# Performance work log

Measured on AMD Instinct MI355X. Metric: run time of the kernel, lower is better.

## Reference

```python
import jax, jax.numpy as jnp
import numpy as np

N = 50000
E = 500000
R = 8
IN_DIM = 128
HID = 128
NUM_CLASSES = 16
NUM_GRAPHS = 64


def setup_inputs() -> dict:
    key = jax.random.key(0)
    ks = jax.random.split(key, 12)
    x = jax.random.normal(ks[0], (N, IN_DIM), dtype=jnp.float32)
    edge_index = jax.random.randint(ks[1], (2, E), 0, N)
    edge_type = jax.random.randint(ks[2], (E,), 0, R)
    batch = jnp.sort(jax.random.randint(ks[3], (N,), 0, NUM_GRAPHS))
    s = 1.0 / np.sqrt(IN_DIM)
    W1 = jax.random.uniform(ks[4], (R, IN_DIM, HID), minval=-s, maxval=s, dtype=jnp.float32)
    root1 = jax.random.uniform(ks[5], (IN_DIM, HID), minval=-s, maxval=s, dtype=jnp.float32)
    b1 = jnp.zeros((HID,), jnp.float32)
    s2 = 1.0 / np.sqrt(HID)
    W2 = jax.random.uniform(ks[6], (R, HID, HID), minval=-s2, maxval=s2, dtype=jnp.float32)
    root2 = jax.random.uniform(ks[7], (HID, HID), minval=-s2, maxval=s2, dtype=jnp.float32)
    b2 = jnp.zeros((HID,), jnp.float32)
    linW = jax.random.uniform(ks[8], (HID, NUM_CLASSES), minval=-s2, maxval=s2, dtype=jnp.float32)
    linb = jnp.zeros((NUM_CLASSES,), jnp.float32)
    return {"x": x, "edge_index": edge_index, "edge_type": edge_type, "batch": batch,
            "W1": W1, "root1": root1, "b1": b1, "W2": W2, "root2": root2, "b2": b2,
            "linW": linW, "linb": linb}


def rgcn_conv(x, src, dst, rel, W, root, b):
    # Per-relation transform of ALL nodes once: [R, N, H] (avoids per-edge weight gather)
    xW = jnp.einsum('nd,rdh->rnh', x, W)
    msg = xW[rel, src]                      # [E, H] gather per edge
    # PyG RGCNConv default aggr='mean': mean over neighbors per (dst, relation)
    seg = dst * R + rel                     # composite segment id
    cnt = jax.ops.segment_sum(jnp.ones((msg.shape[0],), msg.dtype), seg, num_segments=N * R)
    norm = 1.0 / jnp.maximum(cnt, 1.0)
    msg = msg * norm[seg][:, None]
    agg = jax.ops.segment_sum(msg, dst, num_segments=N)  # sum over relations folds in
    return agg + x @ root + b


def global_mean_pool(x, batch):
    sums = jax.ops.segment_sum(x, batch, num_segments=NUM_GRAPHS)
    cnt = jax.ops.segment_sum(jnp.ones((x.shape[0],), x.dtype), batch, num_segments=NUM_GRAPHS)
    return sums / jnp.maximum(cnt, 1.0)[:, None]


def reference(x, edge_index, edge_type, batch, W1, root1, b1, W2, root2, b2, linW, linb):
    src, dst = edge_index[0], edge_index[1]
    h = jax.nn.relu(rgcn_conv(x, src, dst, edge_type, W1, root1, b1))
    h = jax.nn.relu(rgcn_conv(h, src, dst, edge_type, W2, root2, b2))
    pooled = global_mean_pool(h, batch)     # [G, HID]
    return pooled @ linW + linb             # [G, NUM_CLASSES]
```

## Files before the change

kernel.cpp:

```cpp
#include <hip/hip_runtime.h>
#include <hip/hip_bf16.h>
#include <stdint.h>

#define N_NODES 50000
#define N_EDGES 500000
#define R_REL 8
#define HID 128
#define KIN 128
#define KOUT 1152
#define N8 400000
#define NUM_GRAPHS 64
#define NUM_CLASSES 16

#define BN 32
#define LDA 1160
#define NBLK 1563

typedef __attribute__((ext_vector_type(8))) short bf16x8;
typedef __attribute__((ext_vector_type(4))) float f32x4;

__device__ __forceinline__ uint16_t f2bf(float f) {
  uint32_t u = __float_as_uint(f);
  u += 0x7FFFu + ((u >> 16) & 1u);
  return (uint16_t)(u >> 16);
}
__device__ __forceinline__ float bf2f(uint32_t b) {
  return __uint_as_float(b << 16);
}
__device__ __forceinline__ uint32_t pack2bf(float a, float b) {
  return (uint32_t)f2bf(a) | ((uint32_t)f2bf(b) << 16);
}
#define MFMA(a, b, c) __builtin_amdgcn_mfma_f32_16x16x32_bf16((a), (b), (c), 0, 0, 0)

#define HIST_B 1954
#define BND_B 196
#define WP_B 72
#define CVT_B 3125
__global__ __launch_bounds__(256) void k_prep(const int* __restrict__ ei, const int* __restrict__ et,
                                              int* __restrict__ deg8,
                                              const int* __restrict__ batch,
                                              int* __restrict__ gs, int* __restrict__ ge,
                                              const float* __restrict__ W1, const float* __restrict__ root1,
                                              uint16_t* __restrict__ Wf1,
                                              const float* __restrict__ W2, const float* __restrict__ root2,
                                              uint16_t* __restrict__ Wf2,
                                              const float* __restrict__ x, uint16_t* __restrict__ xb) {
  int b = blockIdx.x;
  int t = threadIdx.x;
  if (b < HIST_B) {
    int i = b * 256 + t;
    if (i < N_EDGES) atomicAdd(&deg8[ei[N_EDGES + i] * R_REL + et[i]], 1);
    return;
  }
  b -= HIST_B;
  if (b < BND_B) {
    int i = b * 256 + t;
    if (i < N_NODES) {
      int g = batch[i];
      if (i == 0) gs[g] = 0;
      else { int pg = batch[i - 1]; if (pg != g) { ge[pg] = i; gs[g] = i; } }
      if (i == N_NODES - 1) ge[g] = N_NODES;
    }
    return;
  }
  b -= BND_B;
  if (b < WP_B) {
    __shared__ float lw[32 * 129];
    const float* W    = (b < 36) ? W1 : W2;
    const float* root = (b < 36) ? root1 : root2;
    uint16_t*    Wf   = (b < 36) ? Wf1 : Wf2;
    int kc = (b < 36) ? b : b - 36;
    #pragma unroll
    for (int j = 0; j < 4; ++j) {
      int fi = j * 256 + t;
      int row = fi >> 5, c4 = fi & 31;
      int kk = kc * 32 + row;
      int s = kk >> 7, k = kk & 127;
      const float* src = (s < R_REL) ? (W + ((size_t)s * KIN + k) * HID) : (root + (size_t)k * HID);
      float4 v = *(const float4*)(src + c4 * 4);
      lw[row * 129 + c4 * 4 + 0] = v.x;
      lw[row * 129 + c4 * 4 + 1] = v.y;
      lw[row * 129 + c4 * 4 + 2] = v.z;
      lw[row * 129 + c4 * 4 + 3] = v.w;
    }
    __syncthreads();
    #pragma unroll
    for (int p = 0; p < 2; ++p) {
      int slot = p * 256 + t;
      int nt = slot >> 6, L = slot & 63;
      int quad = L >> 4, l16 = L & 15;
      uint16_t tmp[8];
      #pragma unroll
      for (int e = 0; e < 8; ++e)
        tmp[e] = f2bf(lw[(quad * 8 + e) * 129 + nt * 16 + l16]);
      uint4 o;
      o.x = (uint32_t)tmp[0] | ((uint32_t)tmp[1] << 16);
      o.y = (uint32_t)tmp[2] | ((uint32_t)tmp[3] << 16);
      o.z = (uint32_t)tmp[4] | ((uint32_t)tmp[5] << 16);
      o.w = (uint32_t)tmp[6] | ((uint32_t)tmp[7] << 16);
      *(uint4*)(Wf + ((size_t)(kc * 8 + nt) * 512 + (size_t)L * 8)) = o;
    }
    return;
  }
  b -= WP_B;
  {
    int i = b * 256 + t;
    const float4* p = (const float4*)x + (size_t)i * 2;
    float4 a = p[0], c = p[1];
    uint4 o;
    o.x = pack2bf(a.x, a.y); o.y = pack2bf(a.z, a.w);
    o.z = pack2bf(c.x, c.y); o.w = pack2bf(c.z, c.w);
    *(uint4*)(xb + (size_t)i * 8) = o;
  }
}

__global__ __launch_bounds__(256) void k_scan1(const int* __restrict__ deg8, int* __restrict__ offs8,
                                               int* __restrict__ bsum) {
  __shared__ int sh[256];
  int t = threadIdx.x;
  int base = blockIdx.x * 1024 + t * 4;
  int v[4]; int s = 0;
  #pragma unroll
  for (int i = 0; i < 4; ++i) { int idx = base + i; v[i] = (idx < N8) ? deg8[idx] : 0; s += v[i]; }
  sh[t] = s;
  __syncthreads();
  for (int d = 1; d < 256; d <<= 1) {
    int add = (t >= d) ? sh[t - d] : 0;
    __syncthreads();
    sh[t] += add;
    __syncthreads();
  }
  int run = sh[t] - s;
  if (t == 255) bsum[blockIdx.x] = sh[255];
  #pragma unroll
  for (int i = 0; i < 4; ++i) { int idx = base + i; if (idx < N8) offs8[idx] = run; run += v[i]; }
}

__global__ __launch_bounds__(256) void k_scan23(int* __restrict__ offs8, int* __restrict__ nxt,
                                                const int* __restrict__ bsum, int nb) {
  __shared__ int red[4];
  int t = threadIdx.x;
  int blk = blockIdx.x >> 2;
  int pre = 0;
  for (int j = t; j < blk; j += 256) pre += bsum[j];
  #pragma unroll
  for (int d = 1; d < 64; d <<= 1) pre += __shfl_xor(pre, d);
  if ((t & 63) == 0) red[t >> 6] = pre;
  __syncthreads();
  int total = red[0] + red[1] + red[2] + red[3];
  int i = blockIdx.x * 256 + t;
  if (i < N8) {
    int o = offs8[i] + total;
    offs8[i] = o;
    nxt[i] = o;
  }
  if (i == 0) offs8[N8] = N_EDGES;
}

__global__ __launch_bounds__(256) void k_scatter(const int* __restrict__ ei, const int* __restrict__ et,
                                                 int* __restrict__ nxt, uint32_t* __restrict__ epack) {
  int i = blockIdx.x * 256 + threadIdx.x;
  if (i < N_EDGES) {
    int rel = et[i];
    int dst = ei[N_EDGES + i];
    int p = atomicAdd(&nxt[dst * R_REL + rel], 1);
    epack[p] = (uint32_t)ei[i] | ((uint32_t)rel << 16) | ((uint32_t)(dst & 31) << 19);
  }
}

template<int MODE>
__global__ __launch_bounds__(1024, 4) void k_fused(const uint16_t* __restrict__ hin,
                                                   const uint32_t* __restrict__ epack,
                                                   const int* __restrict__ offs8,
                                                   const uint16_t* __restrict__ Wf,
                                                   const float* __restrict__ bias,
                                                   void* __restrict__ hout,
                                                   float* __restrict__ psum,
                                                   const int* __restrict__ batch) {
  __shared__ __align__(16) uint16_t As[BN * LDA];
  int t = threadIdx.x;
  int w = __builtin_amdgcn_readfirstlane(t >> 6);
  int L = t & 63;
  int quad = L >> 4, l16 = L & 15;
  int node0 = blockIdx.x * BN;
  int voff = 2 * L;
  int nt = w & 7, kh = w >> 3;

  {
    bf16x8 z = 0;
    #pragma unroll
    for (int i = 0; i < 4; ++i) ((bf16x8*)As)[i * 1024 + t] = z;
    if (t < 544) ((bf16x8*)As)[4 * 1024 + t] = z;
  }

  const uint16_t* wpk = Wf + ((size_t)(kh * 18 * 8 + nt)) * 512 + (size_t)L * 8;
  bf16x8 b0 = *(const bf16x8*)(wpk);
  bf16x8 b1 = *(const bf16x8*)(wpk + 4096);

  __syncthreads();

  #pragma unroll
  for (int ni = 0; ni < 2; ++ni) {
    int r = w * 2 + ni;
    int n = node0 + r;
    if (n < N_NODES)
      *(uint32_t*)(As + (size_t)r * LDA + R_REL * HID + voff) =
          *(const uint32_t*)(hin + (size_t)n * HID + voff);
  }

  {
    int s0 = offs8[(size_t)node0 * R_REL];
    int s1 = offs8[(size_t)min(node0 + BN, N_NODES) * R_REL];
    int ce = s1 - s0;
    int e0 = s0 + ((ce * w) >> 4);
    int e1 = s0 + ((ce * (w + 1)) >> 4);
    uint32_t kskip = 0xFFFFFFFEu;
    if (e0 > s0) kskip = epack[e0 - 1] >> 16;
    uint32_t cur = 0xFFFFFFFFu;
    float ax = 0.f, ay = 0.f; int ct = 0;
    bool done = false;
    int lsel = L & 15;
    uint32_t pv = epack[e0 + lsel];
    #pragma unroll 1
    for (int g = e0; g < s1 && !done; g += 16) {
      uint32_t pc = pv;
      int m = min(16, s1 - g);
      pv = epack[g + 16 + lsel];
      uint32_t sv[16], vv[16];
      #pragma unroll
      for (int i = 0; i < 16; ++i)
        sv[i] = (uint32_t)__builtin_amdgcn_readlane((int)pc, i);
      #pragma unroll
      for (int i = 0; i < 16; ++i) {
        uint32_t src = sv[i] & 0xFFFFu;
        src = (src < (uint32_t)N_NODES) ? src : 0u;
        vv[i] = *(const uint32_t*)(hin + (size_t)src * HID + voff);
      }
      #pragma unroll
      for (int i = 0; i < 16; ++i) {
        if (i >= m) break;
        uint32_t k = sv[i] >> 16;
        if (k == cur) {
          uint32_t v = vv[i];
          ax += bf2f(v & 0xFFFFu); ay += bf2f(v >> 16); ++ct;
        } else if (k != kskip) {
          if (cur != 0xFFFFFFFFu) {
            float iv = __builtin_amdgcn_rcpf((float)ct);
            *(uint32_t*)(As + (size_t)(cur >> 3) * LDA + (cur & 7u) * HID + voff) =
                pack2bf(ax * iv, ay * iv);
          }
          if (g + i >= e1) { done = true; cur = 0xFFFFFFFFu; break; }
          cur = k;
          uint32_t v = vv[i];
          ax = bf2f(v & 0xFFFFu); ay = bf2f(v >> 16); ct = 1;
        }
      }
    }
    if (cur != 0xFFFFFFFFu) {
      float iv = __builtin_amdgcn_rcpf((float)ct);
      *(uint32_t*)(As + (size_t)(cur >> 3) * LDA + (cur & 7u) * HID + voff) =
          pack2bf(ax * iv, ay * iv);
    }
  }
  __syncthreads();

  f32x4 acc0 = (f32x4){0.f, 0.f, 0.f, 0.f};
  f32x4 acc1 = (f32x4){0.f, 0.f, 0.f, 0.f};
  {
    const uint16_t* apk = As + (size_t)l16 * LDA + quad * 8 + kh * 18 * 32;
    bf16x8 a00 = *(const bf16x8*)(apk);
    bf16x8 a01 = *(const bf16x8*)(apk + 16 * LDA);
    #pragma unroll 1
    for (int kc = 0; kc < 16; kc += 2) {
      bf16x8 nb0 = *(const bf16x8*)(wpk + (size_t)(kc + 2) * 4096);
      bf16x8 na0 = *(const bf16x8*)(apk + (kc + 1) * 32);
      bf16x8 na1 = *(const bf16x8*)(apk + (kc + 1) * 32 + 16 * LDA);
      acc0 = MFMA(a00, b0, acc0);
      acc1 = MFMA(a01, b0, acc1);
      b0 = nb0;
      bf16x8 nb1 = *(const bf16x8*)(wpk + (size_t)(kc + 3) * 4096);
      bf16x8 ma0 = *(const bf16x8*)(apk + (kc + 2) * 32);
      bf16x8 ma1 = *(const bf16x8*)(apk + (kc + 2) * 32 + 16 * LDA);
      acc0 = MFMA(na0, b1, acc0);
      acc1 = MFMA(na1, b1, acc1);
      b1 = nb1; a00 = ma0; a01 = ma1;
    }
    bf16x8 ta0 = *(const bf16x8*)(apk + 17 * 32);
    bf16x8 ta1 = *(const bf16x8*)(apk + 17 * 32 + 16 * LDA);
    acc0 = MFMA(a00, b0, acc0);
    acc1 = MFMA(a01, b0, acc1);
    acc0 = MFMA(ta0, b1, acc0);
    acc1 = MFMA(ta1, b1, acc1);
  }

  float* scratch = (float*)As;
  __syncthreads();
  if (kh == 1) {
    float* sp = scratch + (size_t)(nt * 2) * 256 + L * 4;
    *(f32x4*)(sp) = acc0;
    *(f32x4*)(sp + 256) = acc1;
  }
  __syncthreads();
  if (kh == 0) {
    const float* sp = scratch + (size_t)(nt * 2) * 256 + L * 4;
    acc0 += *(const f32x4*)(sp);
    acc1 += *(const f32x4*)(sp + 256);

    int col = nt * 16 + l16;
    float bv = bias[col];
    if (MODE == 0) {
      #pragma unroll
      for (int rg = 0; rg < 4; ++rg) {
        int row = node0 + quad * 4 + rg;
        if (row < N_NODES)
          ((uint16_t*)hout)[(size_t)row * HID + col] = f2bf(fmaxf(acc0[rg] + bv, 0.f));
      }
      #pragma unroll
      for (int rg = 0; rg < 4; ++rg) {
        int row = node0 + 16 + quad * 4 + rg;
        if (row < N_NODES)
          ((uint16_t*)hout)[(size_t)row * HID + col] = f2bf(fmaxf(acc1[rg] + bv, 0.f));
      }
    } else {
      bool fast = false;
      int gA = 0;
      if (node0 + BN <= N_NODES) {
        gA = batch[node0];
        int gB = batch[node0 + BN - 1];
        fast = (gA == gB);
      }
      if (fast) {
        float s = 0.f;
        #pragma unroll
        for (int rg = 0; rg < 4; ++rg) s += fmaxf(acc0[rg] + bv, 0.f);
        #pragma unroll
        for (int rg = 0; rg < 4; ++rg) s += fmaxf(acc1[rg] + bv, 0.f);
        s += __shfl_xor(s, 16);
        s += __shfl_xor(s, 32);
        if (quad == 0) atomicAdd(&psum[gA * HID + col], s);
      } else {
        int gp = -1; float run = 0.f;
        #pragma unroll
        for (int k = 0; k < 8; ++k) {
          int rg = k & 3;
          int row = node0 + (k >> 2) * 16 + quad * 4 + rg;
          float v = (k < 4) ? acc0[rg] : acc1[rg];
          if (row < N_NODES) {
            int gg = batch[row];
            if (gg != gp) {
              if (gp >= 0) atomicAdd(&psum[gp * HID + col], run);
              run = 0.f; gp = gg;
            }
            run += fmaxf(v + bv, 0.f);
          }
        }
        if (gp >= 0) atomicAdd(&psum[gp * HID + col], run);
      }
    }
  }
}

__global__ __launch_bounds__(1024) void k_final(const float* __restrict__ psum,
                                                const int* __restrict__ gs, const int* __restrict__ ge,
                                                const float* __restrict__ linW, const float* __restrict__ linb,
                                                float* __restrict__ out) {
  __shared__ float lp[NUM_GRAPHS * HID];
  __shared__ float lw[HID * NUM_CLASSES];
  int i = threadIdx.x;
  #pragma unroll
  for (int j = 0; j < 8; ++j) lp[j * 1024 + i] = psum[j * 1024 + i];
  #pragma unroll
  for (int j = 0; j < 2; ++j) lw[j * 1024 + i] = linW[j * 1024 + i];
  __syncthreads();
  int g = i >> 4, c = i & 15;
  float inv = 1.f / fmaxf((float)(ge[g] - gs[g]), 1.f);
  float s = 0.f;
  #pragma unroll 8
  for (int k = 0; k < HID; ++k) s += lp[g * HID + k] * lw[k * NUM_CLASSES + c];
  out[i] = s * inv + linb[c];
}

extern "C" void kernel_launch(void* const* d_in, const int* in_sizes, int n_in,
                              void* d_out, int out_size, void* d_ws, size_t ws_size,
                              hipStream_t stream) {
  const float* x     = (const float*)d_in[0];
  const int*   ei    = (const int*)d_in[1];
  const int*   et    = (const int*)d_in[2];
  const int*   batch = (const int*)d_in[3];
  const float* W1    = (const float*)d_in[4];
  const float* root1 = (const float*)d_in[5];
  const float* b1    = (const float*)d_in[6];
  const float* W2    = (const float*)d_in[7];
  const float* root2 = (const float*)d_in[8];
  const float* b2    = (const float*)d_in[9];
  const float* linW  = (const float*)d_in[10];
  const float* linb  = (const float*)d_in[11];
  float* out = (float*)d_out;

  char* ws = (char*)d_ws;
  size_t off = 0;
  auto alloc = [&](size_t bytes) -> char* {
    char* p = ws + off;
    off += (bytes + 255) & ~(size_t)255;
    return p;
  };
  int*      deg8  = (int*)alloc((size_t)N8 * 4);
  int*      gb    = (int*)alloc(2 * NUM_GRAPHS * 4);
  float*    psum  = (float*)alloc((size_t)NUM_GRAPHS * HID * 4);
  size_t zbytes = (size_t)N8 * 4 + 512 + (size_t)NUM_GRAPHS * HID * 4;
  int*      gs    = gb;
  int*      ge    = gb + NUM_GRAPHS;
  int*      offs8 = (int*)alloc((size_t)(N8 + 1) * 4);
  int*      nxt   = (int*)alloc((size_t)N8 * 4);
  int*      bsum  = (int*)alloc(512 * 4);
  uint32_t* epack = (uint32_t*)alloc((size_t)(N_EDGES + 64) * 4);
  uint16_t* Wf1   = (uint16_t*)alloc((size_t)KOUT * KIN * 2);
  uint16_t* Wf2   = (uint16_t*)alloc((size_t)KOUT * KIN * 2);
  uint16_t* xb    = (uint16_t*)alloc((size_t)N_NODES * HID * 2);
  uint16_t* h1b   = (uint16_t*)alloc((size_t)N_NODES * HID * 2);

  hipMemsetAsync(deg8, 0, zbytes, stream);

  int nb = (N8 + 1023) / 1024;
  k_prep<<<HIST_B + BND_B + WP_B + CVT_B, 256, 0, stream>>>(
      ei, et, deg8, batch, gs, ge, W1, root1, Wf1, W2, root2, Wf2, x, xb);
  k_scan1<<<nb, 256, 0, stream>>>(deg8, offs8, bsum);
  k_scan23<<<(N8 + 255) / 256, 256, 0, stream>>>(offs8, nxt, bsum, nb);
  k_scatter<<<(N_EDGES + 255) / 256, 256, 0, stream>>>(ei, et, nxt, epack);

  k_fused<0><<<NBLK, 1024, 0, stream>>>(xb,  epack, offs8, Wf1, b1, h1b, nullptr, nullptr);
  k_fused<1><<<NBLK, 1024, 0, stream>>>(h1b, epack, offs8, Wf2, b2, nullptr, psum, batch);

  k_final<<<1, 1024, 0, stream>>>(psum, gs, ge, linW, linb, out);
}
```

Measured before the change: 267.7 us.

## Double node tile per block, widen MFMA tiling, fuse scan, double-buffer edge gathers

Each fused block now processes 64 nodes instead of 32. Waves are re-split into 4 K-slices × 2 column halves × 2 row halves, each computing a 2×4 grid of MFMA tiles, so every loaded weight fragment is reused across more rows. The two-pass scan is merged into one kernel that claims block bases with a global atomic and writes per-tile end offsets. The neighbor gather is double-buffered so one batch of loads is in flight while the previous batch is reduced. The larger LDS tile (about 148KB) lowers how many blocks fit per CU. Scan block order also becomes nondeterministic, so edge layout can differ between runs.

Measured after the change: 355.8 us. 1.33x slower.

```diff
diff --git a/kernel.cpp b/kernel.cpp
--- a/kernel.cpp
+++ b/kernel.cpp
@@ -12,9 +12,9 @@
 #define NUM_GRAPHS 64
 #define NUM_CLASSES 16
 
-#define BN 32
+#define BN 64
 #define LDA 1160
-#define NBLK 1563
+#define NBLK 782
 
 typedef __attribute__((ext_vector_type(8))) short bf16x8;
 typedef __attribute__((ext_vector_type(4))) float f32x4;
@@ -114,9 +114,11 @@
   }
 }
 
-__global__ __launch_bounds__(256) void k_scan1(const int* __restrict__ deg8, int* __restrict__ offs8,
-                                               int* __restrict__ bsum) {
+__global__ __launch_bounds__(256) void k_scan(const int* __restrict__ deg8, int* __restrict__ offs8,
+                                              int* __restrict__ nxt, int* __restrict__ ends,
+                                              int* __restrict__ gcount) {
   __shared__ int sh[256];
+  __shared__ int base_sh;
   int t = threadIdx.x;
   int base = blockIdx.x * 1024 + t * 4;
   int v[4]; int s = 0;
@@ -130,31 +132,18 @@
     sh[t] += add;
     __syncthreads();
   }
-  int run = sh[t] - s;
-  if (t == 255) bsum[blockIdx.x] = sh[255];
-  #pragma unroll
-  for (int i = 0; i < 4; ++i) { int idx = base + i; if (idx < N8) offs8[idx] = run; run += v[i]; }
-}
-
-__global__ __launch_bounds__(256) void k_scan23(int* __restrict__ offs8, int* __restrict__ nxt,
-                                                const int* __restrict__ bsum, int nb) {
-  __shared__ int red[4];
-  int t = threadIdx.x;
-  int blk = blockIdx.x >> 2;
-  int pre = 0;
-  for (int j = t; j < blk; j += 256) pre += bsum[j];
-  #pragma unroll
-  for (int d = 1; d < 64; d <<= 1) pre += __shfl_xor(pre, d);
-  if ((t & 63) == 0) red[t >> 6] = pre;
-  __syncthreads();
-  int total = red[0] + red[1] + red[2] + red[3];
-  int i = blockIdx.x * 256 + t;
-  if (i < N8) {
-    int o = offs8[i] + total;
-    offs8[i] = o;
-    nxt[i] = o;
-  }
-  if (i == 0) offs8[N8] = N_EDGES;
+  if (t == 0) base_sh = atomicAdd(gcount, sh[255]);
+  __syncthreads();
+  int gbase = base_sh;
+  int run = gbase + sh[t] - s;
+  #pragma unroll
+  for (int i = 0; i < 4; ++i) {
+    int idx = base + i;
+    if (idx < N8) { offs8[idx] = run; nxt[idx] = run; }
+    run += v[i];
+  }
+  if (t == 127) ends[2 * blockIdx.x] = gbase + sh[127];
+  if (t == 255) ends[2 * blockIdx.x + 1] = gbase + sh[255];
 }
 
 __global__ __launch_bounds__(256) void k_scatter(const int* __restrict__ ei, const int* __restrict__ et,
@@ -164,14 +153,53 @@
     int rel = et[i];
     int dst = ei[N_EDGES + i];
     int p = atomicAdd(&nxt[dst * R_REL + rel], 1);
-    epack[p] = (uint32_t)ei[i] | ((uint32_t)rel << 16) | ((uint32_t)(dst & 31) << 19);
-  }
-}
+    epack[p] = (uint32_t)ei[i] | ((uint32_t)rel << 16) | ((uint32_t)(dst & 63) << 19);
+  }
+}
+
+#define EXTGATH(pc, sv, vv)                                                   \
+  {                                                                           \
+    _Pragma("unroll")                                                         \
+    for (int i_ = 0; i_ < 16; ++i_)                                           \
+      sv[i_] = (uint32_t)__builtin_amdgcn_readlane((int)(pc), i_);            \
+    _Pragma("unroll")                                                         \
+    for (int i_ = 0; i_ < 16; ++i_) {                                         \
+      uint32_t s_ = sv[i_] & 0xFFFFu;                                         \
+      s_ = (s_ < (uint32_t)N_NODES) ? s_ : 0u;                                \
+      vv[i_] = *(const uint32_t*)(hin + (size_t)s_ * HID + voff);             \
+    }                                                                         \
+    __builtin_amdgcn_sched_barrier(0);                                        \
+  }
+
+#define PROCESS(sv, vv, gbase_)                                               \
+  {                                                                           \
+    int m_ = min(16, blkEnd - (gbase_));                                      \
+    _Pragma("unroll")                                                         \
+    for (int i_ = 0; i_ < 16; ++i_) {                                         \
+      if (i_ >= m_) break;                                                    \
+      uint32_t k_ = sv[i_] >> 16;                                             \
+      if (k_ == cur) {                                                        \
+        uint32_t v_ = vv[i_];                                                 \
+        ax += bf2f(v_ & 0xFFFFu); ay += bf2f(v_ >> 16); ++ct;                 \
+      } else if (k_ != kskip) {                                               \
+        if (cur != 0xFFFFFFFFu) {                                             \
+          float iv_ = __builtin_amdgcn_rcpf((float)ct);                       \
+          *(uint32_t*)(As + (size_t)(cur >> 3) * LDA + (cur & 7u) * HID + voff) = \
+              pack2bf(ax * iv_, ay * iv_);                                    \
+        }                                                                     \
+        if ((gbase_) + i_ >= e1) { done = true; cur = 0xFFFFFFFFu; break; }   \
+        cur = k_;                                                             \
+        uint32_t v_ = vv[i_];                                                 \
+        ax = bf2f(v_ & 0xFFFFu); ay = bf2f(v_ >> 16); ct = 1;                 \
+      }                                                                       \
+    }                                                                         \
+  }
 
 template<int MODE>
 __global__ __launch_bounds__(1024, 4) void k_fused(const uint16_t* __restrict__ hin,
                                                    const uint32_t* __restrict__ epack,
                                                    const int* __restrict__ offs8,
+                                                   const int* __restrict__ ends,
                                                    const uint16_t* __restrict__ Wf,
                                                    const float* __restrict__ bias,
                                                    void* __restrict__ hout,
@@ -184,24 +212,26 @@
   int quad = L >> 4, l16 = L & 15;
   int node0 = blockIdx.x * BN;
   int voff = 2 * L;
-  int nt = w & 7, kh = w >> 3;
+  int kh = w & 3, nt = (w >> 2) & 1, mh = w >> 3;
 
   {
     bf16x8 z = 0;
     #pragma unroll
-    for (int i = 0; i < 4; ++i) ((bf16x8*)As)[i * 1024 + t] = z;
-    if (t < 544) ((bf16x8*)As)[4 * 1024 + t] = z;
-  }
-
-  const uint16_t* wpk = Wf + ((size_t)(kh * 18 * 8 + nt)) * 512 + (size_t)L * 8;
-  bf16x8 b0 = *(const bf16x8*)(wpk);
-  bf16x8 b1 = *(const bf16x8*)(wpk + 4096);
-
-  __syncthreads();
-
-  #pragma unroll
-  for (int ni = 0; ni < 2; ++ni) {
-    int r = w * 2 + ni;
+    for (int i = 0; i < 9; ++i) ((bf16x8*)As)[i * 1024 + t] = z;
+    if (t < 64) ((bf16x8*)As)[9 * 1024 + t] = z;
+  }
+
+  const uint16_t* wpk = Wf + (size_t)(kh * 72 + nt * 4) * 512 + (size_t)L * 8;
+  bf16x8 bc0 = *(const bf16x8*)(wpk);
+  bf16x8 bc1 = *(const bf16x8*)(wpk + 512);
+  bf16x8 bc2 = *(const bf16x8*)(wpk + 1024);
+  bf16x8 bc3 = *(const bf16x8*)(wpk + 1536);
+
+  __syncthreads();
+
+  #pragma unroll
+  for (int ni = 0; ni < 4; ++ni) {
+    int r = w * 4 + ni;
     int n = node0 + r;
     if (n < N_NODES)
       *(uint32_t*)(As + (size_t)r * LDA + R_REL * HID + voff) =
@@ -209,9 +239,9 @@
   }
 
   {
-    int s0 = offs8[(size_t)node0 * R_REL];
-    int s1 = offs8[(size_t)min(node0 + BN, N_NODES) * R_REL];
-    int ce = s1 - s0;
+    int s0 = offs8[node0 * R_REL];
+    int blkEnd = ends[blockIdx.x];
+    int ce = blkEnd - s0;
     int e0 = s0 + ((ce * w) >> 4);
     int e1 = s0 + ((ce * (w + 1)) >> 4);
     uint32_t kskip = 0xFFFFFFFEu;
@@ -220,41 +250,22 @@
     float ax = 0.f, ay = 0.f; int ct = 0;
     bool done = false;
     int lsel = L & 15;
-    uint32_t pv = epack[e0 + lsel];
-    #pragma unroll 1
-    for (int g = e0; g < s1 && !done; g += 16) {
-      uint32_t pc = pv;
-      int m = min(16, s1 - g);
-      pv = epack[g + 16 + lsel];
-      uint32_t sv[16], vv[16];
-      #pragma unroll
-      for (int i = 0; i < 16; ++i)
-        sv[i] = (uint32_t)__builtin_amdgcn_readlane((int)pc, i);
-      #pragma unroll
-      for (int i = 0; i < 16; ++i) {
-        uint32_t src = sv[i] & 0xFFFFu;
-        src = (src < (uint32_t)N_NODES) ? src : 0u;
-        vv[i] = *(const uint32_t*)(hin + (size_t)src * HID + voff);
-      }
-      #pragma unroll
-      for (int i = 0; i < 16; ++i) {
-        if (i >= m) break;
-        uint32_t k = sv[i] >> 16;
-        if (k == cur) {
-          uint32_t v = vv[i];
-          ax += bf2f(v & 0xFFFFu); ay += bf2f(v >> 16); ++ct;
-        } else if (k != kskip) {
-          if (cur != 0xFFFFFFFFu) {
-            float iv = __builtin_amdgcn_rcpf((float)ct);
-            *(uint32_t*)(As + (size_t)(cur >> 3) * LDA + (cur & 7u) * HID + voff) =
-                pack2bf(ax * iv, ay * iv);
-          }
-          if (g + i >= e1) { done = true; cur = 0xFFFFFFFFu; break; }
-          cur = k;
-          uint32_t v = vv[i];
-          ax = bf2f(v & 0xFFFFu); ay = bf2f(v >> 16); ct = 1;
-        }
-      }
+    uint32_t svA[16], vvA[16], svB[16], vvB[16];
+    uint32_t pvA = epack[e0 + lsel];
+    uint32_t pvB = epack[e0 + 16 + lsel];
+    EXTGATH(pvA, svA, vvA);
+    pvA = epack[e0 + 32 + lsel];
+    int g = e0;
+    while (g < blkEnd && !done) {
+      EXTGATH(pvB, svB, vvB);
+      pvB = epack[g + 48 + lsel];
+      PROCESS(svA, vvA, g);
+      g += 16;
+      if (g >= blkEnd || done) break;
+      EXTGATH(pvA, svA, vvA);
+      pvA = epack[g + 48 + lsel];
+      PROCESS(svB, vvB, g);
+      g += 16;
     }
     if (cur != 0xFFFFFFFFu) {
       float iv = __builtin_amdgcn_rcpf((float)ct);
@@ -264,97 +275,125 @@
   }
   __syncthreads();
 
-  f32x4 acc0 = (f32x4){0.f, 0.f, 0.f, 0.f};
-  f32x4 acc1 = (f32x4){0.f, 0.f, 0.f, 0.f};
+  f32x4 acc[2][4];
+  #pragma unroll
+  for (int m = 0; m < 2; ++m)
+    #pragma unroll
+    for (int j = 0; j < 4; ++j) acc[m][j] = (f32x4){0.f, 0.f, 0.f, 0.f};
   {
-    const uint16_t* apk = As + (size_t)l16 * LDA + quad * 8 + kh * 18 * 32;
-    bf16x8 a00 = *(const bf16x8*)(apk);
-    bf16x8 a01 = *(const bf16x8*)(apk + 16 * LDA);
+    const uint16_t* apk = As + (size_t)(mh * 32 + l16) * LDA + quad * 8 + kh * 9 * 32;
     #pragma unroll 1
-    for (int kc = 0; kc < 16; kc += 2) {
-      bf16x8 nb0 = *(const bf16x8*)(wpk + (size_t)(kc + 2) * 4096);
-      bf16x8 na0 = *(const bf16x8*)(apk + (kc + 1) * 32);
-      bf16x8 na1 = *(const bf16x8*)(apk + (kc + 1) * 32 + 16 * LDA);
-      acc0 = MFMA(a00, b0, acc0);
-      acc1 = MFMA(a01, b0, acc1);
-      b0 = nb0;
-      bf16x8 nb1 = *(const bf16x8*)(wpk + (size_t)(kc + 3) * 4096);
-      bf16x8 ma0 = *(const bf16x8*)(apk + (kc + 2) * 32);
-      bf16x8 ma1 = *(const bf16x8*)(apk + (kc + 2) * 32 + 16 * LDA);
-      acc0 = MFMA(na0, b1, acc0);
-      acc1 = MFMA(na1, b1, acc1);
-      b1 = nb1; a00 = ma0; a01 = ma1;
-    }
-    bf16x8 ta0 = *(const bf16x8*)(apk + 17 * 32);
-    bf16x8 ta1 = *(const bf16x8*)(apk + 17 * 32 + 16 * LDA);
-    acc0 = MFMA(a00, b0, acc0);
-    acc1 = MFMA(a01, b0, acc1);
-    acc0 = MFMA(ta0, b1, acc0);
-    acc1 = MFMA(ta1, b1, acc1);
+    for (int kc = 0; kc < 9; ++kc) {
+      int kn = (kc < 8) ? kc + 1 : 8;
+      const uint16_t* wn = wpk + (size_t)kn * 4096;
+      bf16x8 bn0 = *(const bf16x8*)(wn);
+      bf16x8 bn1 = *(const bf16x8*)(wn + 512);
+      bf16x8 bn2 = *(const bf16x8*)(wn + 1024);
+      bf16x8 bn3 = *(const bf16x8*)(wn + 1536);
+      bf16x8 a0 = *(const bf16x8*)(apk + kc * 32);
+      bf16x8 a1 = *(const bf16x8*)(apk + kc * 32 + 16 * LDA);
+      acc[0][0] = MFMA(a0, bc0, acc[0][0]);
+      acc[0][1] = MFMA(a0, bc1, acc[0][1]);
+      acc[0][2] = MFMA(a0, bc2, acc[0][2]);
+      acc[0][3] = MFMA(a0, bc3, acc[0][3]);
+      acc[1][0] = MFMA(a1, bc0, acc[1][0]);
+      acc[1][1] = MFMA(a1, bc1, acc[1][1]);
+      acc[1][2] = MFMA(a1, bc2, acc[1][2]);
+      acc[1][3] = MFMA(a1, bc3, acc[1][3]);
+      bc0 = bn0; bc1 = bn1; bc2 = bn2; bc3 = bn3;
+    }
   }
 
   float* scratch = (float*)As;
   __syncthreads();
-  if (kh == 1) {
-    float* sp = scratch + (size_t)(nt * 2) * 256 + L * 4;
-    *(f32x4*)(sp) = acc0;
-    *(f32x4*)(sp + 256) = acc1;
+  if (kh != 0) {
+    float* sp = scratch + (size_t)(kh - 1) * 8192;
+    #pragma unroll
+    for (int m = 0; m < 2; ++m)
+      #pragma unroll
+      for (int j = 0; j < 4; ++j)
+        *(f32x4*)(sp + (size_t)((mh * 2 + m) * 8 + nt * 4 + j) * 256 + L * 4) = acc[m][j];
   }
   __syncthreads();
   if (kh == 0) {
-    const float* sp = scratch + (size_t)(nt * 2) * 256 + L * 4;
-    acc0 += *(const f32x4*)(sp);
-    acc1 += *(const f32x4*)(sp + 256);
-
-    int col = nt * 16 + l16;
-    float bv = bias[col];
+    #pragma unroll
+    for (int c = 0; c < 3; ++c) {
+      const float* sp = scratch + (size_t)c * 8192;
+      #pragma unroll
+      for (int m = 0; m < 2; ++m)
+        #pragma unroll
+        for (int j = 0; j < 4; ++j)
+          acc[m][j] += *(const f32x4*)(sp + (size_t)((mh * 2 + m) * 8 + nt * 4 + j) * 256 + L * 4);
+    }
+
     if (MODE == 0) {
       #pragma unroll
-      for (int rg = 0; rg < 4; ++rg) {
-        int row = node0 + quad * 4 + rg;
-        if (row < N_NODES)
-          ((uint16_t*)hout)[(size_t)row * HID + col] = f2bf(fmaxf(acc0[rg] + bv, 0.f));
-      }
-      #pragma unroll
-      for (int rg = 0; rg < 4; ++rg) {
-        int row = node0 + 16 + quad * 4 + rg;
-        if (row < N_NODES)
-          ((uint16_t*)hout)[(size_t)row * HID + col] = f2bf(fmaxf(acc1[rg] + bv, 0.f));
+      for (int j = 0; j < 4; ++j) {
+        int col = nt * 64 + j * 16 + l16;
+        float bv = bias[col];
+        #pragma unroll
+        for (int m = 0; m < 2; ++m) {
+          #pragma unroll
+          for (int rg = 0; rg < 4; ++rg) {
+            int row = node0 + mh * 32 + m * 16 + quad * 4 + rg;
+            if (row < N_NODES)
+              ((uint16_t*)hout)[(size_t)row * HID + col] = f2bf(fmaxf(acc[m][j][rg] + bv, 0.f));
+          }
+        }
       }
     } else {
       bool fast = false;
       int gA = 0;
       if (node0 + BN <= N_NODES) {
         gA = batch[node0];
-        int gB = batch[node0 + BN - 1];
-        fast = (gA == gB);
+        fast = (batch[node0 + BN - 1] == gA);
       }
       if (fast) {
-        float s = 0.f;
         #pragma unroll
-        for (int rg = 0; rg < 4; ++rg) s += fmaxf(acc0[rg] + bv, 0.f);
-        #pragma unroll
-        for (int rg = 0; rg < 4; ++rg) s += fmaxf(acc1[rg] + bv, 0.f);
-        s += __shfl_xor(s, 16);
-        s += __shfl_xor(s, 32);
-        if (quad == 0) atomicAdd(&psum[gA * HID + col], s);
+        for (int j = 0; j < 4; ++j) {
+          int col = nt * 64 + j * 16 + l16;
+          float bv = bias[col];
+          float s = 0.f;
+          #pragma unroll
+          for (int m = 0; m < 2; ++m)
+            #pragma unroll
+            for (int rg = 0; rg < 4; ++rg) s += fmaxf(acc[m][j][rg] + bv, 0.f);
+          s += __shfl_xor(s, 16);
+          s += __shfl_xor(s, 32);
+          if (quad == 0) atomicAdd(&psum[gA * HID + col], s);
+        }
       } else {
-        int gp = -1; float run = 0.f;
+        int colb = nt * 64 + l16;
+        float bv0 = bias[colb], bv1 = bias[colb + 16], bv2 = bias[colb + 32], bv3 = bias[colb + 48];
+        int gp = -1;
+        float r0 = 0.f, r1 = 0.f, r2 = 0.f, r3 = 0.f;
         #pragma unroll
         for (int k = 0; k < 8; ++k) {
-          int rg = k & 3;
-          int row = node0 + (k >> 2) * 16 + quad * 4 + rg;
-          float v = (k < 4) ? acc0[rg] : acc1[rg];
+          int m = k >> 2, rg = k & 3;
+          int row = node0 + mh * 32 + m * 16 + quad * 4 + rg;
           if (row < N_NODES) {
             int gg = batch[row];
             if (gg != gp) {
-              if (gp >= 0) atomicAdd(&psum[gp * HID + col], run);
-              run = 0.f; gp = gg;
+              if (gp >= 0) {
+                atomicAdd(&psum[gp * HID + colb],      r0);
+                atomicAdd(&psum[gp * HID + colb + 16], r1);
+                atomicAdd(&psum[gp * HID + colb + 32], r2);
+                atomicAdd(&psum[gp * HID + colb + 48], r3);
+              }
+              r0 = r1 = r2 = r3 = 0.f; gp = gg;
             }
-            run += fmaxf(v + bv, 0.f);
+            r0 += fmaxf(acc[m][0][rg] + bv0, 0.f);
+            r1 += fmaxf(acc[m][1][rg] + bv1, 0.f);
+            r2 += fmaxf(acc[m][2][rg] + bv2, 0.f);
+            r3 += fmaxf(acc[m][3][rg] + bv3, 0.f);
           }
         }
-        if (gp >= 0) atomicAdd(&psum[gp * HID + col], run);
+        if (gp >= 0) {
+          atomicAdd(&psum[gp * HID + colb],      r0);
+          atomicAdd(&psum[gp * HID + colb + 16], r1);
+          atomicAdd(&psum[gp * HID + colb + 32], r2);
+          atomicAdd(&psum[gp * HID + colb + 48], r3);
+        }
       }
     }
   }
@@ -404,16 +443,17 @@
     off += (bytes + 255) & ~(size_t)255;
     return p;
   };
-  int*      deg8  = (int*)alloc((size_t)N8 * 4);
-  int*      gb    = (int*)alloc(2 * NUM_GRAPHS * 4);
-  float*    psum  = (float*)alloc((size_t)NUM_GRAPHS * HID * 4);
-  size_t zbytes = (size_t)N8 * 4 + 512 + (size_t)NUM_GRAPHS * HID * 4;
+  int*      deg8   = (int*)alloc((size_t)N8 * 4);
+  int*      gb     = (int*)alloc(2 * NUM_GRAPHS * 4);
+  float*    psum   = (float*)alloc((size_t)NUM_GRAPHS * HID * 4);
+  int*      gcount = (int*)alloc(4);
+  size_t zbytes = (size_t)N8 * 4 + 512 + (size_t)NUM_GRAPHS * HID * 4 + 256;
   int*      gs    = gb;
   int*      ge    = gb + NUM_GRAPHS;
-  int*      offs8 = (int*)alloc((size_t)(N8 + 1) * 4);
+  int*      offs8 = (int*)alloc((size_t)N8 * 4);
   int*      nxt   = (int*)alloc((size_t)N8 * 4);
-  int*      bsum  = (int*)alloc(512 * 4);
-  uint32_t* epack = (uint32_t*)alloc((size_t)(N_EDGES + 64) * 4);
+  int*      ends  = (int*)alloc((size_t)NBLK * 4);
+  uint32_t* epack = (uint32_t*)alloc((size_t)(N_EDGES + 80) * 4);
   uint16_t* Wf1   = (uint16_t*)alloc((size_t)KOUT * KIN * 2);
   uint16_t* Wf2   = (uint16_t*)alloc((size_t)KOUT * KIN * 2);
   uint16_t* xb    = (uint16_t*)alloc((size_t)N_NODES * HID * 2);
@@ -424,12 +464,11 @@
   int nb = (N8 + 1023) / 1024;
   k_prep<<<HIST_B + BND_B + WP_B + CVT_B, 256, 0, stream>>>(
       ei, et, deg8, batch, gs, ge, W1, root1, Wf1, W2, root2, Wf2, x, xb);
-  k_scan1<<<nb, 256, 0, stream>>>(deg8, offs8, bsum);
-  k_scan23<<<(N8 + 255) / 256, 256, 0, stream>>>(offs8, nxt, bsum, nb);
+  k_scan<<<nb, 256, 0, stream>>>(deg8, offs8, nxt, ends, gcount);
   k_scatter<<<(N_EDGES + 255) / 256, 256, 0, stream>>>(ei, et, nxt, epack);
 
-  k_fused<0><<<NBLK, 1024, 0, stream>>>(xb,  epack, offs8, Wf1, b1, h1b, nullptr, nullptr);
-  k_fused<1><<<NBLK, 1024, 0, stream>>>(h1b, epack, offs8, Wf2, b2, nullptr, psum, batch);
+  k_fused<0><<<NBLK, 1024, 0, stream>>>(xb,  epack, offs8, ends, Wf1, b1, h1b, nullptr, nullptr);
+  k_fused<1><<<NBLK, 1024, 0, stream>>>(h1b, epack, offs8, ends, Wf2, b2, nullptr, psum, batch);
 
   k_final<<<1, 1024, 0, stream>>>(psum, gs, ge, linW, linb, out);
 }
```

## Merge scan kernels via atomic block bases and double-buffer edge gathers

Applied to the files above, without the earlier changes.

The two-kernel prefix scan becomes a single kernel. Each block claims its base offset with an atomicAdd on a global counter, so blocks are laid out in arbitrary order. It also writes per-fused-block end offsets, which the aggregation kernel now uses instead of the next node's offset. The edge gather loop in the fused kernel is double-buffered: the next 16 neighbor rows are loaded while the current batch is reduced, to hide gather latency. The trade-offs are higher register pressure and segment placement that depends on block scheduling order.

New measurement: 327.0 us. 22.2% more time.

```diff
diff --git a/kernel.cpp b/kernel.cpp
--- a/kernel.cpp
+++ b/kernel.cpp
@@ -114,9 +114,11 @@
   }
 }
 
-__global__ __launch_bounds__(256) void k_scan1(const int* __restrict__ deg8, int* __restrict__ offs8,
-                                               int* __restrict__ bsum) {
+__global__ __launch_bounds__(256) void k_scan(const int* __restrict__ deg8, int* __restrict__ offs8,
+                                              int* __restrict__ nxt, int* __restrict__ ends,
+                                              int* __restrict__ gcount) {
   __shared__ int sh[256];
+  __shared__ int base_sh;
   int t = threadIdx.x;
   int base = blockIdx.x * 1024 + t * 4;
   int v[4]; int s = 0;
@@ -130,31 +132,20 @@
     sh[t] += add;
     __syncthreads();
   }
-  int run = sh[t] - s;
-  if (t == 255) bsum[blockIdx.x] = sh[255];
+  if (t == 0) base_sh = atomicAdd(gcount, sh[255]);
+  __syncthreads();
+  int gbase = base_sh;
+  int run = gbase + sh[t] - s;
   #pragma unroll
-  for (int i = 0; i < 4; ++i) { int idx = base + i; if (idx < N8) offs8[idx] = run; run += v[i]; }
-}
-
-__global__ __launch_bounds__(256) void k_scan23(int* __restrict__ offs8, int* __restrict__ nxt,
-                                                const int* __restrict__ bsum, int nb) {
-  __shared__ int red[4];
-  int t = threadIdx.x;
-  int blk = blockIdx.x >> 2;
-  int pre = 0;
-  for (int j = t; j < blk; j += 256) pre += bsum[j];
-  #pragma unroll
-  for (int d = 1; d < 64; d <<= 1) pre += __shfl_xor(pre, d);
-  if ((t & 63) == 0) red[t >> 6] = pre;
-  __syncthreads();
-  int total = red[0] + red[1] + red[2] + red[3];
-  int i = blockIdx.x * 256 + t;
-  if (i < N8) {
-    int o = offs8[i] + total;
-    offs8[i] = o;
-    nxt[i] = o;
-  }
-  if (i == 0) offs8[N8] = N_EDGES;
+  for (int i = 0; i < 4; ++i) {
+    int idx = base + i;
+    if (idx < N8) { offs8[idx] = run; nxt[idx] = run; }
+    run += v[i];
+  }
+  if ((t & 63) == 63) {
+    int fb = 4 * blockIdx.x + (t >> 6);
+    if (fb < NBLK) ends[fb] = gbase + sh[t];
+  }
 }
 
 __global__ __launch_bounds__(256) void k_scatter(const int* __restrict__ ei, const int* __restrict__ et,
@@ -168,10 +159,49 @@
   }
 }
 
+#define EXTGATH(pc, sv, vv)                                                   \
+  {                                                                           \
+    _Pragma("unroll")                                                         \
+    for (int i_ = 0; i_ < 16; ++i_)                                           \
+      sv[i_] = (uint32_t)__builtin_amdgcn_readlane((int)(pc), i_);            \
+    _Pragma("unroll")                                                         \
+    for (int i_ = 0; i_ < 16; ++i_) {                                         \
+      uint32_t s_ = sv[i_] & 0xFFFFu;                                         \
+      s_ = (s_ < (uint32_t)N_NODES) ? s_ : 0u;                                \
+      vv[i_] = *(const uint32_t*)(hin + (size_t)s_ * HID + voff);             \
+    }                                                                         \
+    __builtin_amdgcn_sched_barrier(0);                                        \
+  }
+
+#define PROCESS(sv, vv, gbase_)                                               \
+  {                                                                           \
+    int m_ = min(16, blkEnd - (gbase_));                                      \
+    _Pragma("unroll")                                                         \
+    for (int i_ = 0; i_ < 16; ++i_) {                                         \
+      if (i_ >= m_) break;                                                    \
+      uint32_t k_ = sv[i_] >> 16;                                             \
+      if (k_ == cur) {                                                        \
+        uint32_t v_ = vv[i_];                                                 \
+        ax += bf2f(v_ & 0xFFFFu); ay += bf2f(v_ >> 16); ++ct;                 \
+      } else if (k_ != kskip) {                                               \
+        if (cur != 0xFFFFFFFFu) {                                             \
+          float iv_ = __builtin_amdgcn_rcpf((float)ct);                       \
+          *(uint32_t*)(As + (size_t)(cur >> 3) * LDA + (cur & 7u) * HID + voff) = \
+              pack2bf(ax * iv_, ay * iv_);                                    \
+        }                                                                     \
+        if ((gbase_) + i_ >= e1) { done = true; cur = 0xFFFFFFFFu; break; }   \
+        cur = k_;                                                             \
+        uint32_t v_ = vv[i_];                                                 \
+        ax = bf2f(v_ & 0xFFFFu); ay = bf2f(v_ >> 16); ct = 1;                 \
+      }                                                                       \
+    }                                                                         \
+  }
+
 template<int MODE>
 __global__ __launch_bounds__(1024, 4) void k_fused(const uint16_t* __restrict__ hin,
                                                    const uint32_t* __restrict__ epack,
                                                    const int* __restrict__ offs8,
+                                                   const int* __restrict__ ends,
                                                    const uint16_t* __restrict__ Wf,
                                                    const float* __restrict__ bias,
                                                    void* __restrict__ hout,
@@ -209,9 +239,9 @@
   }
 
   {
-    int s0 = offs8[(size_t)node0 * R_REL];
-    int s1 = offs8[(size_t)min(node0 + BN, N_NODES) * R_REL];
-    int ce = s1 - s0;
+    int s0 = offs8[node0 * R_REL];
+    int blkEnd = ends[blockIdx.x];
+    int ce = blkEnd - s0;
     int e0 = s0 + ((ce * w) >> 4);
     int e1 = s0 + ((ce * (w + 1)) >> 4);
     uint32_t kskip = 0xFFFFFFFEu;
@@ -220,41 +250,22 @@
     float ax = 0.f, ay = 0.f; int ct = 0;
     bool done = false;
     int lsel = L & 15;
-    uint32_t pv = epack[e0 + lsel];
-    #pragma unroll 1
-    for (int g = e0; g < s1 && !done; g += 16) {
-      uint32_t pc = pv;
-      int m = min(16, s1 - g);
-      pv = epack[g + 16 + lsel];
-      uint32_t sv[16], vv[16];
-      #pragma unroll
-      for (int i = 0; i < 16; ++i)
-        sv[i] = (uint32_t)__builtin_amdgcn_readlane((int)pc, i);
-      #pragma unroll
-      for (int i = 0; i < 16; ++i) {
-        uint32_t src = sv[i] & 0xFFFFu;
-        src = (src < (uint32_t)N_NODES) ? src : 0u;
-        vv[i] = *(const uint32_t*)(hin + (size_t)src * HID + voff);
-      }
-      #pragma unroll
-      for (int i = 0; i < 16; ++i) {
-        if (i >= m) break;
-        uint32_t k = sv[i] >> 16;
-        if (k == cur) {
-          uint32_t v = vv[i];
-          ax += bf2f(v & 0xFFFFu); ay += bf2f(v >> 16); ++ct;
-        } else if (k != kskip) {
-          if (cur != 0xFFFFFFFFu) {
-            float iv = __builtin_amdgcn_rcpf((float)ct);
-            *(uint32_t*)(As + (size_t)(cur >> 3) * LDA + (cur & 7u) * HID + voff) =
-                pack2bf(ax * iv, ay * iv);
-          }
-          if (g + i >= e1) { done = true; cur = 0xFFFFFFFFu; break; }
-          cur = k;
-          uint32_t v = vv[i];
-          ax = bf2f(v & 0xFFFFu); ay = bf2f(v >> 16); ct = 1;
-        }
-      }
+    uint32_t svA[16], vvA[16], svB[16], vvB[16];
+    uint32_t pvA = epack[e0 + lsel];
+    uint32_t pvB = epack[e0 + 16 + lsel];
+    EXTGATH(pvA, svA, vvA);
+    pvA = epack[e0 + 32 + lsel];
+    int g = e0;
+    while (g < blkEnd && !done) {
+      EXTGATH(pvB, svB, vvB);
+      pvB = epack[g + 48 + lsel];
+      PROCESS(svA, vvA, g);
+      g += 16;
+      if (g >= blkEnd || done) break;
+      EXTGATH(pvA, svA, vvA);
+      pvA = epack[g + 48 + lsel];
+      PROCESS(svB, vvB, g);
+      g += 16;
     }
     if (cur != 0xFFFFFFFFu) {
       float iv = __builtin_amdgcn_rcpf((float)ct);
@@ -326,8 +337,7 @@
       int gA = 0;
       if (node0 + BN <= N_NODES) {
         gA = batch[node0];
-        int gB = batch[node0 + BN - 1];
-        fast = (gA == gB);
+        fast = (batch[node0 + BN - 1] == gA);
       }
       if (fast) {
         float s = 0.f;
@@ -404,16 +414,17 @@
     off += (bytes + 255) & ~(size_t)255;
     return p;
   };
-  int*      deg8  = (int*)alloc((size_t)N8 * 4);
-  int*      gb    = (int*)alloc(2 * NUM_GRAPHS * 4);
-  float*    psum  = (float*)alloc((size_t)NUM_GRAPHS * HID * 4);
-  size_t zbytes = (size_t)N8 * 4 + 512 + (size_t)NUM_GRAPHS * HID * 4;
+  int*      deg8   = (int*)alloc((size_t)N8 * 4);
+  int*      gb     = (int*)alloc(2 * NUM_GRAPHS * 4);
+  float*    psum   = (float*)alloc((size_t)NUM_GRAPHS * HID * 4);
+  int*      gcount = (int*)alloc(4);
+  size_t zbytes = (size_t)N8 * 4 + 512 + (size_t)NUM_GRAPHS * HID * 4 + 256;
   int*      gs    = gb;
   int*      ge    = gb + NUM_GRAPHS;
-  int*      offs8 = (int*)alloc((size_t)(N8 + 1) * 4);
+  int*      offs8 = (int*)alloc((size_t)N8 * 4);
   int*      nxt   = (int*)alloc((size_t)N8 * 4);
-  int*      bsum  = (int*)alloc(512 * 4);
-  uint32_t* epack = (uint32_t*)alloc((size_t)(N_EDGES + 64) * 4);
+  int*      ends  = (int*)alloc((size_t)NBLK * 4);
+  uint32_t* epack = (uint32_t*)alloc((size_t)(N_EDGES + 80) * 4);
   uint16_t* Wf1   = (uint16_t*)alloc((size_t)KOUT * KIN * 2);
   uint16_t* Wf2   = (uint16_t*)alloc((size_t)KOUT * KIN * 2);
   uint16_t* xb    = (uint16_t*)alloc((size_t)N_NODES * HID * 2);
@@ -424,12 +435,11 @@
   int nb = (N8 + 1023) / 1024;
   k_prep<<<HIST_B + BND_B + WP_B + CVT_B, 256, 0, stream>>>(
       ei, et, deg8, batch, gs, ge, W1, root1, Wf1, W2, root2, Wf2, x, xb);
-  k_scan1<<<nb, 256, 0, stream>>>(deg8, offs8, bsum);
-  k_scan23<<<(N8 + 255) / 256, 256, 0, stream>>>(offs8, nxt, bsum, nb);
+  k_scan<<<nb, 256, 0, stream>>>(deg8, offs8, nxt, ends, gcount);
   k_scatter<<<(N_EDGES + 255) / 256, 256, 0, stream>>>(ei, et, nxt, epack);
 
-  k_fused<0><<<NBLK, 1024, 0, stream>>>(xb,  epack, offs8, Wf1, b1, h1b, nullptr, nullptr);
-  k_fused<1><<<NBLK, 1024, 0, stream>>>(h1b, epack, offs8, Wf2, b2, nullptr, psum, batch);
+  k_fused<0><<<NBLK, 1024, 0, stream>>>(xb,  epack, offs8, ends, Wf1, b1, h1b, nullptr, nullptr);
+  k_fused<1><<<NBLK, 1024, 0, stream>>>(h1b, epack, offs8, ends, Wf2, b2, nullptr, psum, batch);
 
   k_final<<<1, 1024, 0, stream>>>(psum, gs, ge, linW, linb, out);
 }
```
